# Performance work log

Measured on AMD Instinct MI355X. Metric: run time of the kernel, lower is better.

## Reference

```python
import jax, jax.numpy as jnp
import numpy as np

N_BLOCKS = 2
C = 64
N_HEADS = 4
FF = 256
NB_SEQ = 40
SEQ_LEN = 512
NB_PAIRS = (NB_SEQ * (NB_SEQ - 1)) // 2  # 780
B = 2
EPS_ATT = 1e-6


def _ln(x, g, b, eps=1e-5):
    # LayerNorm over last axis (channels)
    mu = jnp.mean(x, axis=-1, keepdims=True)
    var = jnp.var(x, axis=-1, keepdims=True)
    return (x - mu) * jax.lax.rsqrt(var + eps) * g + b


def _kernel_attn(x, wq, bq, wk, bk, wv, bv, wp, bp):
    # x: [B, M, T, C]; faithful to KernelAxialMultiAttention.
    Bs, M, T, Cc = x.shape
    N, D = N_HEADS, Cc // N_HEADS
    q = jax.nn.elu(x @ wq.T + bq) + 1.0
    k = jax.nn.elu(x @ wk.T + bk) + 1.0
    v = x @ wv.T + bv
    q = q.reshape(Bs, M, T, N, D)
    k = k.reshape(Bs, M, T, N, D)
    v = v.reshape(Bs, M, T, N, D)
    ksum = k.sum(axis=2)                                   # [B,M,N,D]
    z = 1.0 / (jnp.einsum('bmtnd,bmnd->bmtn', q, ksum) + EPS_ATT)  # [B,M,T,N]
    ktv = jnp.einsum('bmtnd,bmtne->bmnde', k, v)           # [B,M,N,D,D]
    # Original does Z.expand(...,T,D) @ KtV where Z's D columns are identical,
    # which equals z * column-sum of KtV (sum over first D axis).
    ktv_cs = ktv.sum(axis=-2)                              # [B,M,N,D]
    V = z[..., None] * ktv_cs[:, :, None, :, :]            # [B,M,T,N,D]
    V = V.reshape(Bs, M, T, Cc)
    return V @ wp.T + bp


def setup_inputs() -> dict:
    key = jax.random.key(0)
    ks = iter(jax.random.split(key, 64))

    def w(shape, scale=0.05):
        return jax.random.normal(next(ks), shape, dtype=jnp.float32) * scale

    # seq2pair gather matrix [P, S]
    ii, jj = np.triu_indices(NB_SEQ, 1)
    sp = np.zeros((NB_PAIRS, NB_SEQ), np.float32)
    sp[np.arange(NB_PAIRS), ii] = 1.0
    sp[np.arange(NB_PAIRS), jj] = 1.0

    inp = {
        'x': jax.random.normal(next(ks), (B, 22, SEQ_LEN, NB_SEQ), dtype=jnp.float32),
        'w_in': w((C, 22)), 'b_in': jnp.zeros((C,), jnp.float32),
        'g0': jnp.ones((C,), jnp.float32), 'be0': jnp.zeros((C,), jnp.float32),
        'rqw': w((N_BLOCKS, C, C)), 'rqb': jnp.zeros((N_BLOCKS, C), jnp.float32),
        'rkw': w((N_BLOCKS, C, C)), 'rkb': jnp.zeros((N_BLOCKS, C), jnp.float32),
        'rvw': w((N_BLOCKS, C, C)), 'rvb': jnp.zeros((N_BLOCKS, C), jnp.float32),
        'rpw': w((N_BLOCKS, C, C)), 'rpb': jnp.zeros((N_BLOCKS, C), jnp.float32),
        'cqw': w((N_BLOCKS, C, C)), 'cqb': jnp.zeros((N_BLOCKS, C), jnp.float32),
        'ckw': w((N_BLOCKS, C, C)), 'ckb': jnp.zeros((N_BLOCKS, C), jnp.float32),
        'cvw': w((N_BLOCKS, C, C)), 'cvb': jnp.zeros((N_BLOCKS, C), jnp.float32),
        'cpw': w((N_BLOCKS, C, C)), 'cpb': jnp.zeros((N_BLOCKS, C), jnp.float32),
        'ln_g': jnp.ones((N_BLOCKS, C), jnp.float32), 'ln_b': jnp.zeros((N_BLOCKS, C), jnp.float32),
        'f1w': w((N_BLOCKS, FF, C)), 'f1b': jnp.zeros((N_BLOCKS, FF), jnp.float32),
        'f2w': w((N_BLOCKS, C, FF)), 'f2b': jnp.zeros((N_BLOCKS, C), jnp.float32),
        'wout': w((1, C)), 'bout': jnp.zeros((1,), jnp.float32),
        'seq2pair': jnp.asarray(sp),
    }
    return inp


def reference(x, w_in, b_in, g0, be0, rqw, rqb, rkw, rkb, rvw, rvb, rpw, rpb,
              cqw, cqb, ckw, ckb, cvw, cvb, cpw, cpb, ln_g, ln_b,
              f1w, f1b, f2w, f2b, wout, bout, seq2pair):
    # block_1_1: 1x1 conv (22->64) + ReLU; x: [B,22,L,S] -> h: [B,C,L,S]
    h = jax.nn.relu(jnp.einsum('bcls,dc->bdls', x, w_in) + b_in[None, :, None, None])
    # seq2pair gather-sum: [B,P,L,C] channel-last representation
    hp = jnp.einsum('ps,bdls->bpld', seq2pair, h)
    hp = _ln(hp, g0, be0)
    for i in range(N_BLOCKS):
        # row attention over seq_len axis (M=P, T=L)
        att = _kernel_attn(hp, rqw[i], rqb[i], rkw[i], rkb[i], rvw[i], rvb[i], rpw[i], rpb[i])
        hp = att + hp
        hp = _ln(hp, ln_g[i], ln_b[i])
        # column attention over pairs axis (M=L, T=P)
        hc = jnp.swapaxes(hp, 1, 2)  # [B,L,P,C]
        att = _kernel_attn(hc, cqw[i], cqb[i], ckw[i], ckb[i], cvw[i], cvb[i], cpw[i], cpb[i])
        hp = jnp.swapaxes(att, 1, 2) + hp
        hp = _ln(hp, ln_g[i], ln_b[i])
        # FFN: 1x1 conv 64->256 GELU 256->64, residual
        f = jax.nn.gelu(hp @ f1w[i].T + f1b[i], approximate=False)
        hp = (f @ f2w[i].T + f2b[i]) + hp
        if i != N_BLOCKS - 1:
            hp = _ln(hp, ln_g[i], ln_b[i])
    # pwFNN: 1x1 conv 64->1 + Softplus, then mean over seq_len axis
    y = jax.nn.softplus(hp @ wout.T + bout)[..., 0]   # [B,P,L]
    return jnp.mean(y, axis=-1)                        # [B,P]
```

## Files before the change

kernel.cpp:

```cpp
#include <hip/hip_runtime.h>
#include <math.h>
#include <stdint.h>

#define B_   2
#define S_   40
#define P_   780
#define L_   512
#define C_   64
#define FF_  256
#define NTOK (B_*P_*L_)

typedef __attribute__((ext_vector_type(8))) short short8;
typedef __attribute__((ext_vector_type(4))) float f32x4;
typedef __attribute__((ext_vector_type(4))) unsigned short us4;

__device__ __forceinline__ float ln64(float r, float g, float b) {
    float s1 = r, s2 = r * r;
    #pragma unroll
    for (int m = 1; m < 64; m <<= 1) {
        s1 += __shfl_xor(s1, m, 64);
        s2 += __shfl_xor(s2, m, 64);
    }
    float mu  = s1 * (1.0f / 64.0f);
    float var = s2 * (1.0f / 64.0f) - mu * mu;
    return (r - mu) * rsqrtf(var + 1e-5f) * g + b;
}
__device__ __forceinline__ float gelu_fast(float x) {
    float x2 = x * x;
    float u  = x * fmaf(0.044715f, x2, 1.0f);
    float e  = __builtin_amdgcn_exp2f(u * 2.302265106f);
    return x * e * __builtin_amdgcn_rcpf(e + 1.0f);
}
__device__ __forceinline__ float softplus_f(float v) {
    return (v > 20.0f) ? v : log1pf(__expf(v));
}
__device__ __forceinline__ float elup1(float v) {
    return (v > 0.0f) ? v + 1.0f : __expf(v);
}
__device__ __forceinline__ unsigned short f2bf(float f) {
    union { float f; uint32_t u; } cv; cv.f = f;
    uint32_t u = cv.u;
    return (unsigned short)((u + 0x7FFFu + ((u >> 16) & 1u)) >> 16);
}
__device__ __forceinline__ float bf2f(unsigned short u) {
    union { uint32_t u; float f; } cv; cv.u = (uint32_t)u << 16; return cv.f;
}
__device__ __forceinline__ uint32_t cvtpk(float a, float b) {
    uint32_t d;
    asm("v_cvt_pk_bf16_f32 %0, %1, %2" : "=v"(d) : "v"(a), "v"(b));
    return d;
}

__global__ void k_conv_in(const float* __restrict__ x, const float* __restrict__ w_in,
                          const float* __restrict__ b_in, float* __restrict__ h) {
    int gid = blockIdx.x * 256 + threadIdx.x;
    int c  = gid & 63;
    int tk = gid >> 6;
    if (tk >= B_ * L_ * S_) return;
    int b = tk / (L_ * S_);
    int r = tk % (L_ * S_);
    int l = r / S_;
    int s = r % S_;
    float acc = b_in[c];
    const float* xb = x + (size_t)b * 22 * L_ * S_ + (size_t)l * S_ + s;
    #pragma unroll
    for (int cc = 0; cc < 22; cc++)
        acc = fmaf(xb[(size_t)cc * L_ * S_], w_in[c * 22 + cc], acc);
    h[gid] = fmaxf(acc, 0.0f);
}

__global__ void k_gather_ln(const float* __restrict__ h, const float* __restrict__ g0,
                            const float* __restrict__ be0, unsigned short* __restrict__ hp) {
    int lane = threadIdx.x & 63;
    int wv   = threadIdx.x >> 6;
    int tk = blockIdx.x * 4 + wv;
    if (tk >= NTOK) return;
    int b = tk / (P_ * L_);
    int r = tk % (P_ * L_);
    int p = r / L_;
    int l = r % L_;
    int i = 0, rem = p, cnt = S_ - 1;
    while (rem >= cnt) { rem -= cnt; cnt--; i++; }
    int j = i + 1 + rem;
    const float* hb = h + (((size_t)b * L_ + l) * S_) * 64;
    float v = hb[i * 64 + lane] + hb[j * 64 + lane];
    hp[(size_t)tk * 64 + lane] = f2bf(ln64(v, g0[lane], be0[lane]));
}

__global__ void k_wprep_qkv(const float* __restrict__ rqw, const float* __restrict__ rkw,
                            const float* __restrict__ rvw, const float* __restrict__ cqw,
                            const float* __restrict__ ckw, const float* __restrict__ cvw,
                            unsigned short* __restrict__ qkvf) {
    int g = blockIdx.x * 256 + threadIdx.x;
    if (g >= 6144) return;
    int m = g >> 9, r = g & 511;
    int mat = m >> 1, layer = m & 1;
    int q = r >> 6, lane = r & 63;
    int c = lane & 15, hi = lane >> 4;
    int nt = q >> 1, s = q & 1;
    const float* base;
    switch (mat) {
        case 0: base = rqw; break; case 1: base = rkw; break; case 2: base = rvw; break;
        case 3: base = cqw; break; case 4: base = ckw; break; default: base = cvw; break;
    }
    const float* src = base + layer * 4096 + (nt * 16 + c) * 64 + s * 32 + hi * 8;
    short8 v;
    #pragma unroll
    for (int i = 0; i < 8; i++) v[i] = (short)f2bf(src[i]);
    *(short8*)(qkvf + (size_t)m * 4096 + (size_t)r * 8) = v;
}

template <bool ROW>
__global__ __launch_bounds__(512) void k_attn_red(
        const unsigned short* __restrict__ xb, const unsigned short* __restrict__ wkf,
        const unsigned short* __restrict__ wvf, const float* __restrict__ bk,
        const float* __restrict__ bv, const float* __restrict__ wp,
        float* __restrict__ stats) {
    __shared__ float redK[8][64];
    __shared__ float redV[8][64];
    __shared__ float kvfin[64];

    const int tid = threadIdx.x, lane = tid & 63, w8 = tid >> 6;
    const int t = lane & 15, hi = lane >> 4;
    const int slice = blockIdx.x;
    const int T  = ROW ? L_ : P_;
    const int NT = ROW ? 32 : 49;
    const size_t base = (size_t)slice * (size_t)T * 64;

    short8 wkfr[4][2], wvfr[4][2];
    #pragma unroll
    for (int nt = 0; nt < 4; nt++)
        #pragma unroll
        for (int s = 0; s < 2; s++) {
            wkfr[nt][s] = *(const short8*)(wkf + ((size_t)((nt*2+s)*64 + lane)) * 8);
            wvfr[nt][s] = *(const short8*)(wvf + ((size_t)((nt*2+s)*64 + lane)) * 8);
        }
    f32x4 bkL[4], bvL[4];
    #pragma unroll
    for (int nt = 0; nt < 4; nt++) {
        bkL[nt] = *(const f32x4*)(bk + nt * 16 + hi * 4);
        bvL[nt] = *(const f32x4*)(bv + nt * 16 + hi * 4);
    }

    float ks[4][4] = {}, kv[4][4] = {};

    for (int tile = w8; tile < NT; tile += 8) {
        int tok = tile * 16 + t;
        bool valid = ROW || (tok < T);
        int tokc = valid ? tok : (T - 1);
        const unsigned short* src = xb + base + (size_t)tokc * 64;
        short8 xf[2];
        #pragma unroll
        for (int s = 0; s < 2; s++)
            xf[s] = *(const short8*)(src + s * 32 + hi * 8);
        f32x4 aK[4], aV[4];
        #pragma unroll
        for (int nt = 0; nt < 4; nt++) { aK[nt] = (f32x4){0,0,0,0}; aV[nt] = (f32x4){0,0,0,0}; }
        #pragma unroll
        for (int nt = 0; nt < 4; nt++)
            #pragma unroll
            for (int s = 0; s < 2; s++) {
                aK[nt] = __builtin_amdgcn_mfma_f32_16x16x32_bf16(wkfr[nt][s], xf[s], aK[nt], 0, 0, 0);
                aV[nt] = __builtin_amdgcn_mfma_f32_16x16x32_bf16(wvfr[nt][s], xf[s], aV[nt], 0, 0, 0);
            }
        #pragma unroll
        for (int nt = 0; nt < 4; nt++) {
            float kk[4], vv[4];
            #pragma unroll
            for (int r = 0; r < 4; r++) {
                kk[r] = valid ? elup1(aK[nt][r] + bkL[nt][r]) : 0.0f;
                vv[r] = valid ? (aV[nt][r] + bvL[nt][r]) : 0.0f;
            }
            float sp = kk[0] + kk[1] + kk[2] + kk[3];
            sp += __shfl_xor(sp, 16, 64);
            sp += __shfl_xor(sp, 32, 64);
            #pragma unroll
            for (int r = 0; r < 4; r++) { ks[nt][r] += kk[r]; kv[nt][r] += sp * vv[r]; }
        }
    }

    #pragma unroll
    for (int nt = 0; nt < 4; nt++)
        #pragma unroll
        for (int r = 0; r < 4; r++) {
            #pragma unroll
            for (int m = 1; m < 16; m <<= 1) {
                ks[nt][r] += __shfl_xor(ks[nt][r], m, 64);
                kv[nt][r] += __shfl_xor(kv[nt][r], m, 64);
            }
        }
    if (t == 0) {
        #pragma unroll
        for (int nt = 0; nt < 4; nt++)
            #pragma unroll
            for (int r = 0; r < 4; r++) {
                redK[w8][nt * 16 + hi * 4 + r] = ks[nt][r];
                redV[w8][nt * 16 + hi * 4 + r] = kv[nt][r];
            }
    }
    __syncthreads();
    if (tid < 64) {
        float a = 0.0f, b2 = 0.0f;
        #pragma unroll
        for (int w = 0; w < 8; w++) { a += redK[w][tid]; b2 += redV[w][tid]; }
        stats[(size_t)slice * 320 + tid] = a;
        kvfin[tid] = b2;
    }
    __syncthreads();
    if (tid < 256) {
        int c = tid & 63, n = tid >> 6;
        const float* wpr = wp + c * 64 + n * 16;
        float s = 0.0f;
        #pragma unroll
        for (int e = 0; e < 16; e++) s = fmaf(kvfin[n * 16 + e], wpr[e], s);
        stats[(size_t)slice * 320 + 64 + c * 4 + n] = s;
    }
}

__global__ __launch_bounds__(256) void k_attn_map_row(
        const unsigned short* __restrict__ hp, unsigned short* __restrict__ hpT,
        const unsigned short* __restrict__ wqf,
        const float* __restrict__ bq, const float* __restrict__ bp,
        const float* __restrict__ stats, const float* __restrict__ lng,
        const float* __restrict__ lnb) {
    const int tid = threadIdx.x, lane = tid & 63, w4 = tid >> 6;
    const int t = lane & 15, hi = lane >> 4;
    const int slice = blockIdx.x >> 3;
    const int tok = ((blockIdx.x & 7) * 4 + w4) * 16 + t;
    const unsigned short* src = hp + ((size_t)slice * L_ + tok) * 64;

    short8 xf[2];
    #pragma unroll
    for (int s = 0; s < 2; s++)
        xf[s] = *(const short8*)(src + s * 32 + hi * 8);

    f32x4 aQ[4];
    #pragma unroll
    for (int nt = 0; nt < 4; nt++) aQ[nt] = (f32x4){0,0,0,0};
    #pragma unroll
    for (int nt = 0; nt < 4; nt++)
        #pragma unroll
        for (int s = 0; s < 2; s++) {
            short8 wfr = *(const short8*)(wqf + ((size_t)((nt*2+s)*64 + lane)) * 8);
            aQ[nt] = __builtin_amdgcn_mfma_f32_16x16x32_bf16(wfr, xf[s], aQ[nt], 0, 0, 0);
        }

    const float* st = stats + (size_t)slice * 320;
    float z[4];
    #pragma unroll
    for (int nt = 0; nt < 4; nt++) {
        f32x4 bq4 = *(const f32x4*)(bq + nt * 16 + hi * 4);
        f32x4 kS  = *(const f32x4*)(st + nt * 16 + hi * 4);
        float d = 0.0f;
        #pragma unroll
        for (int r = 0; r < 4; r++)
            d = fmaf(elup1(aQ[nt][r] + bq4[r]), kS[r], d);
        d += __shfl_xor(d, 16, 64);
        d += __shfl_xor(d, 32, 64);
        z[nt] = 1.0f / (d + 1e-6f);
    }

    float o[4][4];
    float s1 = 0.0f, s2 = 0.0f;
    #pragma unroll
    for (int nt = 0; nt < 4; nt++) {
        f32x4 bp4 = *(const f32x4*)(bp + nt * 16 + hi * 4);
        us4 xr4 = *(const us4*)(src + nt * 16 + hi * 4);
        #pragma unroll
        for (int r = 0; r < 4; r++) {
            int ch = nt * 16 + hi * 4 + r;
            f32x4 wv4 = *(const f32x4*)(st + 64 + ch * 4);
            float val = z[0] * wv4[0] + z[1] * wv4[1] + z[2] * wv4[2] + z[3] * wv4[3]
                      + bp4[r] + bf2f(xr4[r]);
            o[nt][r] = val;
            s1 += val; s2 += val * val;
        }
    }
    s1 += __shfl_xor(s1, 16, 64);  s1 += __shfl_xor(s1, 32, 64);
    s2 += __shfl_xor(s2, 16, 64);  s2 += __shfl_xor(s2, 32, 64);
    float mu  = s1 * (1.0f / 64.0f);
    float var = s2 * (1.0f / 64.0f) - mu * mu;
    float rs  = rsqrtf(var + 1e-5f);

    const int b = slice / P_, p = slice - b * P_;
    unsigned short* dst = hpT + (((size_t)b * L_ + tok) * P_ + p) * 64;
    #pragma unroll
    for (int nt = 0; nt < 4; nt++) {
        f32x4 g4 = *(const f32x4*)(lng + nt * 16 + hi * 4);
        f32x4 b4 = *(const f32x4*)(lnb + nt * 16 + hi * 4);
        float r0 = (o[nt][0] - mu) * rs * g4[0] + b4[0];
        float r1 = (o[nt][1] - mu) * rs * g4[1] + b4[1];
        float r2 = (o[nt][2] - mu) * rs * g4[2] + b4[2];
        float r3 = (o[nt][3] - mu) * rs * g4[3] + b4[3];
        *(uint2*)(dst + nt * 16 + hi * 4) = make_uint2(cvtpk(r0, r1), cvtpk(r2, r3));
    }
}

__global__ void k_wprep(const float* __restrict__ f1w, const float* __restrict__ f2w,
                        unsigned short* __restrict__ w1s, unsigned short* __restrict__ w2s) {
    int g = blockIdx.x * 256 + threadIdx.x;
    if (g >= 8192) return;
    int layer = g >> 12;
    int rem   = g & 4095;
    int which = rem >> 11;
    int idx   = rem & 2047;
    int l  = idx & 63;
    int q  = idx >> 6;
    int c  = l & 15, hi = l >> 4;
    const float* src;
    unsigned short* dst;
    if (which == 0) {
        int s = q & 1, nt = q >> 1;
        src = f1w + (size_t)layer * 16384 + (nt * 16 + c) * 64 + s * 32 + hi * 8;
        dst = w1s + (size_t)layer * 16384 + (size_t)idx * 8;
    } else {
        int s = q & 7, nt = q >> 3;
        src = f2w + (size_t)layer * 16384 + (nt * 16 + c) * 256 + s * 32 + hi * 8;
        dst = w2s + (size_t)layer * 16384 + (size_t)idx * 8;
    }
    short8 v;
    #pragma unroll
    for (int i = 0; i < 8; i++) v[i] = (short)f2bf(src[i]);
    *(short8*)dst = v;
}

template <int MODE>
__global__ __launch_bounds__(256) void k_cmap_ffn(
        const unsigned short* __restrict__ hpT, unsigned short* __restrict__ hp,
        const unsigned short* __restrict__ wqf,
        const float* __restrict__ bq, const float* __restrict__ bpv,
        const float* __restrict__ stats,
        const unsigned short* __restrict__ w1s, const float* __restrict__ f1b,
        const unsigned short* __restrict__ w2s, const float* __restrict__ f2b,
        const float* __restrict__ lng, const float* __restrict__ lnb,
        const float* __restrict__ wout, const float* __restrict__ bout,
        float* __restrict__ out) {
    __shared__ __align__(16) unsigned char Ylds[4][2048];
    __shared__ __align__(16) unsigned char G2[4][4096];

    const int tid = threadIdx.x, lane = tid & 63, wv = tid >> 6;
    const int c = lane & 15, hi = lane >> 4;
    const int slice = blockIdx.x / 13, tile = blockIdx.x % 13;
    const int b = slice >> 9, l = slice & 511;
    const int p = (tile * 4 + wv) * 16 + c;
    const bool valid = p < P_;
    const int pc = valid ? p : P_ - 1;
    const unsigned short* src = hpT + ((size_t)slice * P_ + pc) * 64;

    short8 xf[2];
    #pragma unroll
    for (int s = 0; s < 2; s++)
        xf[s] = *(const short8*)(src + s * 32 + hi * 8);
    f32x4 aQ[4];
    #pragma unroll
    for (int nt = 0; nt < 4; nt++) aQ[nt] = (f32x4){0,0,0,0};
    #pragma unroll
    for (int nt = 0; nt < 4; nt++)
        #pragma unroll
        for (int s = 0; s < 2; s++) {
            short8 wfr = *(const short8*)(wqf + ((size_t)((nt*2+s)*64 + lane)) * 8);
            aQ[nt] = __builtin_amdgcn_mfma_f32_16x16x32_bf16(wfr, xf[s], aQ[nt], 0, 0, 0);
        }
    const float* st = stats + (size_t)slice * 320;
    float z[4];
    #pragma unroll
    for (int nt = 0; nt < 4; nt++) {
        f32x4 bq4 = *(const f32x4*)(bq + nt * 16 + hi * 4);
        f32x4 kS  = *(const f32x4*)(st + nt * 16 + hi * 4);
        float d = 0.0f;
        #pragma unroll
        for (int r = 0; r < 4; r++)
            d = fmaf(elup1(aQ[nt][r] + bq4[r]), kS[r], d);
        d += __shfl_xor(d, 16, 64);
        d += __shfl_xor(d, 32, 64);
        z[nt] = 1.0f / (d + 1e-6f);
    }

    float vv[4][4];
    {
        float s1 = 0.0f, s2 = 0.0f;
        #pragma unroll
        for (int nt = 0; nt < 4; nt++) {
            f32x4 bp4 = *(const f32x4*)(bpv + nt * 16 + hi * 4);
            us4 xr4 = *(const us4*)(src + nt * 16 + hi * 4);
            #pragma unroll
            for (int r = 0; r < 4; r++) {
                int ch = nt * 16 + hi * 4 + r;
                f32x4 wv4 = *(const f32x4*)(st + 64 + ch * 4);
                float val = z[0] * wv4[0] + z[1] * wv4[1] + z[2] * wv4[2] + z[3] * wv4[3]
                          + bp4[r] + bf2f(xr4[r]);
                vv[nt][r] = val;
                s1 += val; s2 += val * val;
            }
        }
        s1 += __shfl_xor(s1, 16, 64);  s1 += __shfl_xor(s1, 32, 64);
        s2 += __shfl_xor(s2, 16, 64);  s2 += __shfl_xor(s2, 32, 64);
        float mu  = s1 * (1.0f / 64.0f);
        float var = s2 * (1.0f / 64.0f) - mu * mu;
        float rs  = rsqrtf(var + 1e-5f);
        #pragma unroll
        for (int nt = 0; nt < 4; nt++) {
            f32x4 g4 = *(const f32x4*)(lng + nt * 16 + hi * 4);
            f32x4 b4 = *(const f32x4*)(lnb + nt * 16 + hi * 4);
            #pragma unroll
            for (int r = 0; r < 4; r++)
                vv[nt][r] = (vv[nt][r] - mu) * rs * g4[r] + b4[r];
        }
    }

    unsigned char* yw = &Ylds[wv][0];
    #pragma unroll
    for (int nt = 0; nt < 4; nt++) {
        uint2 w = make_uint2(cvtpk(vv[nt][0], vv[nt][1]), cvtpk(vv[nt][2], vv[nt][3]));
        uint32_t ch0 = nt * 16 + hi * 4;
        uint32_t boff = (uint32_t)c * 128 + ((ch0 >> 3) ^ (uint32_t)(c & 7)) * 16 + (ch0 & 7) * 2;
        *(uint2*)(yw + boff) = w;
    }
    short8 xb2[2];
    #pragma unroll
    for (int s = 0; s < 2; s++)
        xb2[s] = *(short8*)(yw + (uint32_t)c * 128 +
                            (((uint32_t)(s * 4 + hi)) ^ (uint32_t)(c & 7)) * 16);

    f32x4 acc2[4];
    #pragma unroll
    for (int n2 = 0; n2 < 4; n2++)
        acc2[n2] = *(const f32x4*)(f2b + n2 * 16 + hi * 4);

    unsigned char* g2w = &G2[wv][0] + c * 256;
    #pragma unroll
    for (int half = 0; half < 2; half++) {
        #pragma unroll
        for (int ntl = 0; ntl < 8; ntl++) {
            int nt = half * 8 + ntl;
            f32x4 acc = *(const f32x4*)(f1b + nt * 16 + hi * 4);
            #pragma unroll
            for (int s = 0; s < 2; s++) {
                short8 wf = *(const short8*)(w1s + ((size_t)(nt * 2 + s) * 64 + lane) * 8);
                acc = __builtin_amdgcn_mfma_f32_16x16x32_bf16(wf, xb2[s], acc, 0, 0, 0);
            }
            uint32_t p0 = cvtpk(gelu_fast(acc[0]), gelu_fast(acc[1]));
            uint32_t p1 = cvtpk(gelu_fast(acc[2]), gelu_fast(acc[3]));
            uint32_t woff = ((uint32_t)(ntl * 32 + hi * 8)) ^ ((uint32_t)(c & 7) << 4);
            *(uint2*)(g2w + woff) = make_uint2(p0, p1);
        }
        #pragma unroll
        for (int sl = 0; sl < 4; sl++) {
            int s = half * 4 + sl;
            uint32_t roff = ((uint32_t)(sl * 64 + hi * 16)) ^ ((uint32_t)(c & 7) << 4);
            short8 fa = *(short8*)(g2w + roff);
            #pragma unroll
            for (int n2 = 0; n2 < 4; n2++) {
                short8 wf = *(const short8*)(w2s + ((size_t)(n2 * 8 + s) * 64 + lane) * 8);
                acc2[n2] = __builtin_amdgcn_mfma_f32_16x16x32_bf16(wf, fa, acc2[n2], 0, 0, 0);
            }
        }
    }

    float vo[4][4];
    float s1 = 0.0f, s2 = 0.0f;
    #pragma unroll
    for (int n2 = 0; n2 < 4; n2++)
        #pragma unroll
        for (int r = 0; r < 4; r++) {
            float v = acc2[n2][r] + vv[n2][r];
            vo[n2][r] = v;
            s1 += v; s2 += v * v;
        }

    if (MODE == 0) {
        s1 += __shfl_xor(s1, 16, 64);  s1 += __shfl_xor(s1, 32, 64);
        s2 += __shfl_xor(s2, 16, 64);  s2 += __shfl_xor(s2, 32, 64);
        float mu  = s1 * (1.0f / 64.0f);
        float var = s2 * (1.0f / 64.0f) - mu * mu;
        float rs  = rsqrtf(var + 1e-5f);
        if (valid) {
            unsigned short* dst = hp + (((size_t)b * P_ + pc) * L_ + l) * 64;
            #pragma unroll
            for (int n2 = 0; n2 < 4; n2++) {
                f32x4 g4 = *(const f32x4*)(lng + n2 * 16 + hi * 4);
                f32x4 b4 = *(const f32x4*)(lnb + n2 * 16 + hi * 4);
                float r0 = (vo[n2][0] - mu) * rs * g4[0] + b4[0];
                float r1 = (vo[n2][1] - mu) * rs * g4[1] + b4[1];
                float r2 = (vo[n2][2] - mu) * rs * g4[2] + b4[2];
                float r3 = (vo[n2][3] - mu) * rs * g4[3] + b4[3];
                *(uint2*)(dst + n2 * 16 + hi * 4) = make_uint2(cvtpk(r0, r1), cvtpk(r2, r3));
            }
        }
    } else {
        float part = 0.0f;
        #pragma unroll
        for (int n2 = 0; n2 < 4; n2++) {
            f32x4 w4 = *(const f32x4*)(wout + n2 * 16 + hi * 4);
            #pragma unroll
            for (int r = 0; r < 4; r++)
                part = fmaf(vo[n2][r], w4[r], part);
        }
        part += __shfl_xor(part, 16, 64);
        part += __shfl_xor(part, 32, 64);
        if (hi == 0 && valid) {
            float sp = softplus_f(part + bout[0]);
            atomicAdd(out + b * P_ + pc, sp * (1.0f / L_));
        }
    }
}

extern "C" void kernel_launch(void* const* d_in, const int* in_sizes, int n_in,
                              void* d_out, int out_size, void* d_ws, size_t ws_size,
                              hipStream_t stream) {
    const float* x    = (const float*)d_in[0];
    const float* w_in = (const float*)d_in[1];
    const float* b_in = (const float*)d_in[2];
    const float* g0   = (const float*)d_in[3];
    const float* be0  = (const float*)d_in[4];
    const float* rqw  = (const float*)d_in[5];  const float* rqb = (const float*)d_in[6];
    const float* rkw  = (const float*)d_in[7];  const float* rkb = (const float*)d_in[8];
    const float* rvw  = (const float*)d_in[9];  const float* rvb = (const float*)d_in[10];
    const float* rpw  = (const float*)d_in[11]; const float* rpb = (const float*)d_in[12];
    const float* cqw  = (const float*)d_in[13]; const float* cqb = (const float*)d_in[14];
    const float* ckw  = (const float*)d_in[15]; const float* ckb = (const float*)d_in[16];
    const float* cvw  = (const float*)d_in[17]; const float* cvb = (const float*)d_in[18];
    const float* cpw  = (const float*)d_in[19]; const float* cpb = (const float*)d_in[20];
    const float* lng  = (const float*)d_in[21]; const float* lnb = (const float*)d_in[22];
    const float* f1w  = (const float*)d_in[23]; const float* f1b = (const float*)d_in[24];
    const float* f2w  = (const float*)d_in[25]; const float* f2b = (const float*)d_in[26];
    const float* wout = (const float*)d_in[27]; const float* bout= (const float*)d_in[28];
    float* out = (float*)d_out;

    unsigned short* hp  = (unsigned short*)d_ws;
    unsigned short* hpT = hp + (size_t)NTOK * 64;
    float* h = (float*)(hpT + (size_t)NTOK * 64);
    unsigned short* w1s  = (unsigned short*)h;
    unsigned short* w2s  = w1s + 2 * 16384;
    unsigned short* qkvf = w2s + 2 * 16384;
    float* stats = (float*)(qkvf + 12 * 4096);

    hipMemsetAsync(out, 0, (size_t)out_size * sizeof(float), stream);

    k_conv_in<<<(B_ * L_ * S_ * 64) / 256, 256, 0, stream>>>(x, w_in, b_in, h);
    k_gather_ln<<<NTOK / 4, 256, 0, stream>>>(h, g0, be0, hp);
    k_wprep<<<32, 256, 0, stream>>>(f1w, f2w, w1s, w2s);
    k_wprep_qkv<<<24, 256, 0, stream>>>(rqw, rkw, rvw, cqw, ckw, cvw, qkvf);

    for (int i = 0; i < 2; i++) {
        k_attn_red<true><<<B_ * P_, 512, 0, stream>>>(hp,
            qkvf + (size_t)(2 + i) * 4096, qkvf + (size_t)(4 + i) * 4096,
            rkb + i * 64, rvb + i * 64, rpw + i * 4096, stats);
        k_attn_map_row<<<B_ * P_ * 8, 256, 0, stream>>>(hp, hpT,
            qkvf + (size_t)(0 + i) * 4096, rqb + i * 64, rpb + i * 64,
            stats, lng + i * 64, lnb + i * 64);
        k_attn_red<false><<<B_ * L_, 512, 0, stream>>>(hpT,
            qkvf + (size_t)(8 + i) * 4096, qkvf + (size_t)(10 + i) * 4096,
            ckb + i * 64, cvb + i * 64, cpw + i * 4096, stats);
        if (i == 0) {
            k_cmap_ffn<0><<<B_ * L_ * 13, 256, 0, stream>>>(hpT, hp,
                qkvf + (size_t)(6 + i) * 4096, cqb + i * 64, cpb + i * 64, stats,
                w1s + (size_t)i * 16384, f1b + i * 256,
                w2s + (size_t)i * 16384, f2b + i * 64,
                lng + i * 64, lnb + i * 64, wout, bout, out);
        } else {
            k_cmap_ffn<1><<<B_ * L_ * 13, 256, 0, stream>>>(hpT, hp,
                qkvf + (size_t)(6 + i) * 4096, cqb + i * 64, cpb + i * 64, stats,
                w1s + (size_t)i * 16384, f1b + i * 256,
                w2s + (size_t)i * 16384, f2b + i * 64,
                lng + i * 64, lnb + i * 64, wout, bout, out);
        }
    }
}
```

Before: 1.175 ms.

## Fuse attention reduction and map passes into single per-slice kernels

Merges the K/V reduction kernel with the Q map kernel for row attention, and the column reduction with the column map plus FFN kernel. Each block now owns a whole slice: it keeps the token fragments in registers (row) or re-reads them (column), reduces the stats into shared memory, and applies the map in the same launch. This removes the global stats round trip, two launches per layer, and a second read of the activations. In exchange, grids become much smaller (1560 and 1024 blocks of 512 threads), register and LDS pressure rises, and each block serializes its reduce and map phases.

```diff
diff --git a/kernel.cpp b/kernel.cpp
--- a/kernel.cpp
+++ b/kernel.cpp
@@ -108,192 +108,6 @@
     #pragma unroll
     for (int i = 0; i < 8; i++) v[i] = (short)f2bf(src[i]);
     *(short8*)(qkvf + (size_t)m * 4096 + (size_t)r * 8) = v;
-}
-
-template <bool ROW>
-__global__ __launch_bounds__(512) void k_attn_red(
-        const unsigned short* __restrict__ xb, const unsigned short* __restrict__ wkf,
-        const unsigned short* __restrict__ wvf, const float* __restrict__ bk,
-        const float* __restrict__ bv, const float* __restrict__ wp,
-        float* __restrict__ stats) {
-    __shared__ float redK[8][64];
-    __shared__ float redV[8][64];
-    __shared__ float kvfin[64];
-
-    const int tid = threadIdx.x, lane = tid & 63, w8 = tid >> 6;
-    const int t = lane & 15, hi = lane >> 4;
-    const int slice = blockIdx.x;
-    const int T  = ROW ? L_ : P_;
-    const int NT = ROW ? 32 : 49;
-    const size_t base = (size_t)slice * (size_t)T * 64;
-
-    short8 wkfr[4][2], wvfr[4][2];
-    #pragma unroll
-    for (int nt = 0; nt < 4; nt++)
-        #pragma unroll
-        for (int s = 0; s < 2; s++) {
-            wkfr[nt][s] = *(const short8*)(wkf + ((size_t)((nt*2+s)*64 + lane)) * 8);
-            wvfr[nt][s] = *(const short8*)(wvf + ((size_t)((nt*2+s)*64 + lane)) * 8);
-        }
-    f32x4 bkL[4], bvL[4];
-    #pragma unroll
-    for (int nt = 0; nt < 4; nt++) {
-        bkL[nt] = *(const f32x4*)(bk + nt * 16 + hi * 4);
-        bvL[nt] = *(const f32x4*)(bv + nt * 16 + hi * 4);
-    }
-
-    float ks[4][4] = {}, kv[4][4] = {};
-
-    for (int tile = w8; tile < NT; tile += 8) {
-        int tok = tile * 16 + t;
-        bool valid = ROW || (tok < T);
-        int tokc = valid ? tok : (T - 1);
-        const unsigned short* src = xb + base + (size_t)tokc * 64;
-        short8 xf[2];
-        #pragma unroll
-        for (int s = 0; s < 2; s++)
-            xf[s] = *(const short8*)(src + s * 32 + hi * 8);
-        f32x4 aK[4], aV[4];
-        #pragma unroll
-        for (int nt = 0; nt < 4; nt++) { aK[nt] = (f32x4){0,0,0,0}; aV[nt] = (f32x4){0,0,0,0}; }
-        #pragma unroll
-        for (int nt = 0; nt < 4; nt++)
-            #pragma unroll
-            for (int s = 0; s < 2; s++) {
-                aK[nt] = __builtin_amdgcn_mfma_f32_16x16x32_bf16(wkfr[nt][s], xf[s], aK[nt], 0, 0, 0);
-                aV[nt] = __builtin_amdgcn_mfma_f32_16x16x32_bf16(wvfr[nt][s], xf[s], aV[nt], 0, 0, 0);
-            }
-        #pragma unroll
-        for (int nt = 0; nt < 4; nt++) {
-            float kk[4], vv[4];
-            #pragma unroll
-            for (int r = 0; r < 4; r++) {
-                kk[r] = valid ? elup1(aK[nt][r] + bkL[nt][r]) : 0.0f;
-                vv[r] = valid ? (aV[nt][r] + bvL[nt][r]) : 0.0f;
-            }
-            float sp = kk[0] + kk[1] + kk[2] + kk[3];
-            sp += __shfl_xor(sp, 16, 64);
-            sp += __shfl_xor(sp, 32, 64);
-            #pragma unroll
-            for (int r = 0; r < 4; r++) { ks[nt][r] += kk[r]; kv[nt][r] += sp * vv[r]; }
-        }
-    }
-
-    #pragma unroll
-    for (int nt = 0; nt < 4; nt++)
-        #pragma unroll
-        for (int r = 0; r < 4; r++) {
-            #pragma unroll
-            for (int m = 1; m < 16; m <<= 1) {
-                ks[nt][r] += __shfl_xor(ks[nt][r], m, 64);
-                kv[nt][r] += __shfl_xor(kv[nt][r], m, 64);
-            }
-        }
-    if (t == 0) {
-        #pragma unroll
-        for (int nt = 0; nt < 4; nt++)
-            #pragma unroll
-            for (int r = 0; r < 4; r++) {
-                redK[w8][nt * 16 + hi * 4 + r] = ks[nt][r];
-                redV[w8][nt * 16 + hi * 4 + r] = kv[nt][r];
-            }
-    }
-    __syncthreads();
-    if (tid < 64) {
-        float a = 0.0f, b2 = 0.0f;
-        #pragma unroll
-        for (int w = 0; w < 8; w++) { a += redK[w][tid]; b2 += redV[w][tid]; }
-        stats[(size_t)slice * 320 + tid] = a;
-        kvfin[tid] = b2;
-    }
-    __syncthreads();
-    if (tid < 256) {
-        int c = tid & 63, n = tid >> 6;
-        const float* wpr = wp + c * 64 + n * 16;
-        float s = 0.0f;
-        #pragma unroll
-        for (int e = 0; e < 16; e++) s = fmaf(kvfin[n * 16 + e], wpr[e], s);
-        stats[(size_t)slice * 320 + 64 + c * 4 + n] = s;
-    }
-}
-
-__global__ __launch_bounds__(256) void k_attn_map_row(
-        const unsigned short* __restrict__ hp, unsigned short* __restrict__ hpT,
-        const unsigned short* __restrict__ wqf,
-        const float* __restrict__ bq, const float* __restrict__ bp,
-        const float* __restrict__ stats, const float* __restrict__ lng,
-        const float* __restrict__ lnb) {
-    const int tid = threadIdx.x, lane = tid & 63, w4 = tid >> 6;
-    const int t = lane & 15, hi = lane >> 4;
-    const int slice = blockIdx.x >> 3;
-    const int tok = ((blockIdx.x & 7) * 4 + w4) * 16 + t;
-    const unsigned short* src = hp + ((size_t)slice * L_ + tok) * 64;
-
-    short8 xf[2];
-    #pragma unroll
-    for (int s = 0; s < 2; s++)
-        xf[s] = *(const short8*)(src + s * 32 + hi * 8);
-
-    f32x4 aQ[4];
-    #pragma unroll
-    for (int nt = 0; nt < 4; nt++) aQ[nt] = (f32x4){0,0,0,0};
-    #pragma unroll
-    for (int nt = 0; nt < 4; nt++)
-        #pragma unroll
-        for (int s = 0; s < 2; s++) {
-            short8 wfr = *(const short8*)(wqf + ((size_t)((nt*2+s)*64 + lane)) * 8);
-            aQ[nt] = __builtin_amdgcn_mfma_f32_16x16x32_bf16(wfr, xf[s], aQ[nt], 0, 0, 0);
-        }
-
-    const float* st = stats + (size_t)slice * 320;
-    float z[4];
-    #pragma unroll
-    for (int nt = 0; nt < 4; nt++) {
-        f32x4 bq4 = *(const f32x4*)(bq + nt * 16 + hi * 4);
-        f32x4 kS  = *(const f32x4*)(st + nt * 16 + hi * 4);
-        float d = 0.0f;
-        #pragma unroll
-        for (int r = 0; r < 4; r++)
-            d = fmaf(elup1(aQ[nt][r] + bq4[r]), kS[r], d);
-        d += __shfl_xor(d, 16, 64);
-        d += __shfl_xor(d, 32, 64);
-        z[nt] = 1.0f / (d + 1e-6f);
-    }
-
-    float o[4][4];
-    float s1 = 0.0f, s2 = 0.0f;
-    #pragma unroll
-    for (int nt = 0; nt < 4; nt++) {
-        f32x4 bp4 = *(const f32x4*)(bp + nt * 16 + hi * 4);
-        us4 xr4 = *(const us4*)(src + nt * 16 + hi * 4);
-        #pragma unroll
-        for (int r = 0; r < 4; r++) {
-            int ch = nt * 16 + hi * 4 + r;
-            f32x4 wv4 = *(const f32x4*)(st + 64 + ch * 4);
-            float val = z[0] * wv4[0] + z[1] * wv4[1] + z[2] * wv4[2] + z[3] * wv4[3]
-                      + bp4[r] + bf2f(xr4[r]);
-            o[nt][r] = val;
-            s1 += val; s2 += val * val;
-        }
-    }
-    s1 += __shfl_xor(s1, 16, 64);  s1 += __shfl_xor(s1, 32, 64);
-    s2 += __shfl_xor(s2, 16, 64);  s2 += __shfl_xor(s2, 32, 64);
-    float mu  = s1 * (1.0f / 64.0f);
-    float var = s2 * (1.0f / 64.0f) - mu * mu;
-    float rs  = rsqrtf(var + 1e-5f);
-
-    const int b = slice / P_, p = slice - b * P_;
-    unsigned short* dst = hpT + (((size_t)b * L_ + tok) * P_ + p) * 64;
-    #pragma unroll
-    for (int nt = 0; nt < 4; nt++) {
-        f32x4 g4 = *(const f32x4*)(lng + nt * 16 + hi * 4);
-        f32x4 b4 = *(const f32x4*)(lnb + nt * 16 + hi * 4);
-        float r0 = (o[nt][0] - mu) * rs * g4[0] + b4[0];
-        float r1 = (o[nt][1] - mu) * rs * g4[1] + b4[1];
-        float r2 = (o[nt][2] - mu) * rs * g4[2] + b4[2];
-        float r3 = (o[nt][3] - mu) * rs * g4[3] + b4[3];
-        *(uint2*)(dst + nt * 16 + hi * 4) = make_uint2(cvtpk(r0, r1), cvtpk(r2, r3));
-    }
 }
 
 __global__ void k_wprep(const float* __restrict__ f1w, const float* __restrict__ f2w,
@@ -324,183 +138,464 @@
     *(short8*)dst = v;
 }
 
+__global__ __launch_bounds__(512) void k_row_fused(
+        const unsigned short* __restrict__ hp, unsigned short* __restrict__ hpT,
+        const unsigned short* __restrict__ wqf, const unsigned short* __restrict__ wkf,
+        const unsigned short* __restrict__ wvf,
+        const float* __restrict__ bq, const float* __restrict__ bk,
+        const float* __restrict__ bv, const float* __restrict__ wp,
+        const float* __restrict__ bp, const float* __restrict__ lng,
+        const float* __restrict__ lnb) {
+    __shared__ float redK[8][64];
+    __shared__ float redV[8][64];
+    __shared__ float kvfin[64];
+    __shared__ float sksum[64];
+    __shared__ float swkv[256];
+
+    const int tid = threadIdx.x, lane = tid & 63, w8 = tid >> 6;
+    const int t = lane & 15, hi = lane >> 4;
+    const int slice = blockIdx.x;
+    const size_t base = (size_t)slice * L_ * 64;
+
+    short8 xkeep[4][2];
+    float ks[4][4] = {}, kv[4][4] = {};
+    {
+        short8 wkfr[4][2], wvfr[4][2];
+        #pragma unroll
+        for (int nt = 0; nt < 4; nt++)
+            #pragma unroll
+            for (int s = 0; s < 2; s++) {
+                wkfr[nt][s] = *(const short8*)(wkf + ((size_t)((nt*2+s)*64 + lane)) * 8);
+                wvfr[nt][s] = *(const short8*)(wvf + ((size_t)((nt*2+s)*64 + lane)) * 8);
+            }
+        f32x4 bkL[4], bvL[4];
+        #pragma unroll
+        for (int nt = 0; nt < 4; nt++) {
+            bkL[nt] = *(const f32x4*)(bk + nt * 16 + hi * 4);
+            bvL[nt] = *(const f32x4*)(bv + nt * 16 + hi * 4);
+        }
+        #pragma unroll
+        for (int it = 0; it < 4; it++) {
+            int tok = (w8 + it * 8) * 16 + t;
+            const unsigned short* src = hp + base + (size_t)tok * 64;
+            #pragma unroll
+            for (int s = 0; s < 2; s++)
+                xkeep[it][s] = *(const short8*)(src + s * 32 + hi * 8);
+            f32x4 aK[4], aV[4];
+            #pragma unroll
+            for (int nt = 0; nt < 4; nt++) { aK[nt] = (f32x4){0,0,0,0}; aV[nt] = (f32x4){0,0,0,0}; }
+            #pragma unroll
+            for (int nt = 0; nt < 4; nt++)
+                #pragma unroll
+                for (int s = 0; s < 2; s++) {
+                    aK[nt] = __builtin_amdgcn_mfma_f32_16x16x32_bf16(wkfr[nt][s], xkeep[it][s], aK[nt], 0, 0, 0);
+                    aV[nt] = __builtin_amdgcn_mfma_f32_16x16x32_bf16(wvfr[nt][s], xkeep[it][s], aV[nt], 0, 0, 0);
+                }
+            #pragma unroll
+            for (int nt = 0; nt < 4; nt++) {
+                float kk[4], vv[4];
+                #pragma unroll
+                for (int r = 0; r < 4; r++) {
+                    kk[r] = elup1(aK[nt][r] + bkL[nt][r]);
+                    vv[r] = aV[nt][r] + bvL[nt][r];
+                }
+                float sp = kk[0] + kk[1] + kk[2] + kk[3];
+                sp += __shfl_xor(sp, 16, 64);
+                sp += __shfl_xor(sp, 32, 64);
+                #pragma unroll
+                for (int r = 0; r < 4; r++) { ks[nt][r] += kk[r]; kv[nt][r] += sp * vv[r]; }
+            }
+        }
+    }
+    #pragma unroll
+    for (int nt = 0; nt < 4; nt++)
+        #pragma unroll
+        for (int r = 0; r < 4; r++) {
+            #pragma unroll
+            for (int m = 1; m < 16; m <<= 1) {
+                ks[nt][r] += __shfl_xor(ks[nt][r], m, 64);
+                kv[nt][r] += __shfl_xor(kv[nt][r], m, 64);
+            }
+        }
+    if (t == 0) {
+        #pragma unroll
+        for (int nt = 0; nt < 4; nt++)
+            #pragma unroll
+            for (int r = 0; r < 4; r++) {
+                redK[w8][nt * 16 + hi * 4 + r] = ks[nt][r];
+                redV[w8][nt * 16 + hi * 4 + r] = kv[nt][r];
+            }
+    }
+    __syncthreads();
+    if (tid < 64) {
+        float a = 0.0f, b2 = 0.0f;
+        #pragma unroll
+        for (int w = 0; w < 8; w++) { a += redK[w][tid]; b2 += redV[w][tid]; }
+        sksum[tid] = a;
+        kvfin[tid] = b2;
+    }
+    __syncthreads();
+    if (tid < 256) {
+        int c = tid & 63, n = tid >> 6;
+        const float* wpr = wp + c * 64 + n * 16;
+        float s = 0.0f;
+        #pragma unroll
+        for (int e = 0; e < 16; e++) s = fmaf(kvfin[n * 16 + e], wpr[e], s);
+        swkv[c * 4 + n] = s;
+    }
+    __syncthreads();
+
+    short8 wqfr[4][2];
+    #pragma unroll
+    for (int nt = 0; nt < 4; nt++)
+        #pragma unroll
+        for (int s = 0; s < 2; s++)
+            wqfr[nt][s] = *(const short8*)(wqf + ((size_t)((nt*2+s)*64 + lane)) * 8);
+    f32x4 bqL[4], bpL[4], gL[4], bL[4];
+    #pragma unroll
+    for (int nt = 0; nt < 4; nt++) {
+        bqL[nt] = *(const f32x4*)(bq + nt * 16 + hi * 4);
+        bpL[nt] = *(const f32x4*)(bp + nt * 16 + hi * 4);
+        gL[nt]  = *(const f32x4*)(lng + nt * 16 + hi * 4);
+        bL[nt]  = *(const f32x4*)(lnb + nt * 16 + hi * 4);
+    }
+    const int bb = slice / P_, pp = slice - bb * P_;
+
+    #pragma unroll
+    for (int it = 0; it < 4; it++) {
+        int tok = (w8 + it * 8) * 16 + t;
+        f32x4 aQ[4];
+        #pragma unroll
+        for (int nt = 0; nt < 4; nt++) aQ[nt] = (f32x4){0,0,0,0};
+        #pragma unroll
+        for (int nt = 0; nt < 4; nt++)
+            #pragma unroll
+            for (int s = 0; s < 2; s++)
+                aQ[nt] = __builtin_amdgcn_mfma_f32_16x16x32_bf16(wqfr[nt][s], xkeep[it][s], aQ[nt], 0, 0, 0);
+        float z[4];
+        #pragma unroll
+        for (int nt = 0; nt < 4; nt++) {
+            f32x4 kS = *(const f32x4*)(sksum + nt * 16 + hi * 4);
+            float d = 0.0f;
+            #pragma unroll
+            for (int r = 0; r < 4; r++)
+                d = fmaf(elup1(aQ[nt][r] + bqL[nt][r]), kS[r], d);
+            d += __shfl_xor(d, 16, 64);
+            d += __shfl_xor(d, 32, 64);
+            z[nt] = 1.0f / (d + 1e-6f);
+        }
+        const unsigned short* srcr = hp + base + (size_t)tok * 64;
+        float o[4][4];
+        float s1 = 0.0f, s2 = 0.0f;
+        #pragma unroll
+        for (int nt = 0; nt < 4; nt++) {
+            us4 xr4 = *(const us4*)(srcr + nt * 16 + hi * 4);
+            #pragma unroll
+            for (int r = 0; r < 4; r++) {
+                int ch = nt * 16 + hi * 4 + r;
+                f32x4 wv4 = *(const f32x4*)(swkv + ch * 4);
+                float val = z[0] * wv4[0] + z[1] * wv4[1] + z[2] * wv4[2] + z[3] * wv4[3]
+                          + bpL[nt][r] + bf2f(xr4[r]);
+                o[nt][r] = val;
+                s1 += val; s2 += val * val;
+            }
+        }
+        s1 += __shfl_xor(s1, 16, 64);  s1 += __shfl_xor(s1, 32, 64);
+        s2 += __shfl_xor(s2, 16, 64);  s2 += __shfl_xor(s2, 32, 64);
+        float mu  = s1 * (1.0f / 64.0f);
+        float var = s2 * (1.0f / 64.0f) - mu * mu;
+        float rs  = rsqrtf(var + 1e-5f);
+        unsigned short* dst = hpT + (((size_t)bb * L_ + tok) * P_ + pp) * 64;
+        #pragma unroll
+        for (int nt = 0; nt < 4; nt++) {
+            float r0 = (o[nt][0] - mu) * rs * gL[nt][0] + bL[nt][0];
+            float r1 = (o[nt][1] - mu) * rs * gL[nt][1] + bL[nt][1];
+            float r2 = (o[nt][2] - mu) * rs * gL[nt][2] + bL[nt][2];
+            float r3 = (o[nt][3] - mu) * rs * gL[nt][3] + bL[nt][3];
+            *(uint2*)(dst + nt * 16 + hi * 4) = make_uint2(cvtpk(r0, r1), cvtpk(r2, r3));
+        }
+    }
+}
+
 template <int MODE>
-__global__ __launch_bounds__(256) void k_cmap_ffn(
+__global__ __launch_bounds__(512) void k_col_fused(
         const unsigned short* __restrict__ hpT, unsigned short* __restrict__ hp,
-        const unsigned short* __restrict__ wqf,
-        const float* __restrict__ bq, const float* __restrict__ bpv,
-        const float* __restrict__ stats,
+        const unsigned short* __restrict__ wqf, const unsigned short* __restrict__ wkf,
+        const unsigned short* __restrict__ wvf,
+        const float* __restrict__ bq, const float* __restrict__ bk,
+        const float* __restrict__ bv, const float* __restrict__ wp,
+        const float* __restrict__ bpv,
         const unsigned short* __restrict__ w1s, const float* __restrict__ f1b,
         const unsigned short* __restrict__ w2s, const float* __restrict__ f2b,
         const float* __restrict__ lng, const float* __restrict__ lnb,
         const float* __restrict__ wout, const float* __restrict__ bout,
         float* __restrict__ out) {
-    __shared__ __align__(16) unsigned char Ylds[4][2048];
-    __shared__ __align__(16) unsigned char G2[4][4096];
-
-    const int tid = threadIdx.x, lane = tid & 63, wv = tid >> 6;
-    const int c = lane & 15, hi = lane >> 4;
-    const int slice = blockIdx.x / 13, tile = blockIdx.x % 13;
-    const int b = slice >> 9, l = slice & 511;
-    const int p = (tile * 4 + wv) * 16 + c;
-    const bool valid = p < P_;
-    const int pc = valid ? p : P_ - 1;
-    const unsigned short* src = hpT + ((size_t)slice * P_ + pc) * 64;
-
-    short8 xf[2];
-    #pragma unroll
-    for (int s = 0; s < 2; s++)
-        xf[s] = *(const short8*)(src + s * 32 + hi * 8);
-    f32x4 aQ[4];
-    #pragma unroll
-    for (int nt = 0; nt < 4; nt++) aQ[nt] = (f32x4){0,0,0,0};
+    __shared__ float redK[8][64];
+    __shared__ float redV[8][64];
+    __shared__ float kvfin[64];
+    __shared__ float sksum[64];
+    __shared__ float swkv[256];
+    __shared__ __align__(16) unsigned char G2[8][4096];
+
+    const int tid = threadIdx.x, lane = tid & 63, w8 = tid >> 6;
+    const int t = lane & 15, hi = lane >> 4;
+    const int slice = blockIdx.x;
+    const int bb = slice >> 9, ll = slice & 511;
+    const size_t base = (size_t)slice * P_ * 64;
+
+    float ks[4][4] = {}, kv[4][4] = {};
+    {
+        short8 wkfr[4][2], wvfr[4][2];
+        #pragma unroll
+        for (int nt = 0; nt < 4; nt++)
+            #pragma unroll
+            for (int s = 0; s < 2; s++) {
+                wkfr[nt][s] = *(const short8*)(wkf + ((size_t)((nt*2+s)*64 + lane)) * 8);
+                wvfr[nt][s] = *(const short8*)(wvf + ((size_t)((nt*2+s)*64 + lane)) * 8);
+            }
+        f32x4 bkL[4], bvL[4];
+        #pragma unroll
+        for (int nt = 0; nt < 4; nt++) {
+            bkL[nt] = *(const f32x4*)(bk + nt * 16 + hi * 4);
+            bvL[nt] = *(const f32x4*)(bv + nt * 16 + hi * 4);
+        }
+        #pragma unroll 1
+        for (int tile = w8; tile < 49; tile += 8) {
+            int tok = tile * 16 + t;
+            bool valid = tok < P_;
+            int tokc = valid ? tok : (P_ - 1);
+            const unsigned short* src = hpT + base + (size_t)tokc * 64;
+            short8 xf[2];
+            #pragma unroll
+            for (int s = 0; s < 2; s++)
+                xf[s] = *(const short8*)(src + s * 32 + hi * 8);
+            f32x4 aK[4], aV[4];
+            #pragma unroll
+            for (int nt = 0; nt < 4; nt++) { aK[nt] = (f32x4){0,0,0,0}; aV[nt] = (f32x4){0,0,0,0}; }
+            #pragma unroll
+            for (int nt = 0; nt < 4; nt++)
+                #pragma unroll
+                for (int s = 0; s < 2; s++) {
+                    aK[nt] = __builtin_amdgcn_mfma_f32_16x16x32_bf16(wkfr[nt][s], xf[s], aK[nt], 0, 0, 0);
+                    aV[nt] = __builtin_amdgcn_mfma_f32_16x16x32_bf16(wvfr[nt][s], xf[s], aV[nt], 0, 0, 0);
+                }
+            #pragma unroll
+            for (int nt = 0; nt < 4; nt++) {
+                float kk[4], vv[4];
+                #pragma unroll
+                for (int r = 0; r < 4; r++) {
+                    kk[r] = valid ? elup1(aK[nt][r] + bkL[nt][r]) : 0.0f;
+                    vv[r] = valid ? (aV[nt][r] + bvL[nt][r]) : 0.0f;
+                }
+                float sp = kk[0] + kk[1] + kk[2] + kk[3];
+                sp += __shfl_xor(sp, 16, 64);
+                sp += __shfl_xor(sp, 32, 64);
+                #pragma unroll
+                for (int r = 0; r < 4; r++) { ks[nt][r] += kk[r]; kv[nt][r] += sp * vv[r]; }
+            }
+        }
+    }
     #pragma unroll
     for (int nt = 0; nt < 4; nt++)
         #pragma unroll
-        for (int s = 0; s < 2; s++) {
-            short8 wfr = *(const short8*)(wqf + ((size_t)((nt*2+s)*64 + lane)) * 8);
-            aQ[nt] = __builtin_amdgcn_mfma_f32_16x16x32_bf16(wfr, xf[s], aQ[nt], 0, 0, 0);
-        }
-    const float* st = stats + (size_t)slice * 320;
-    float z[4];
+        for (int r = 0; r < 4; r++) {
+            #pragma unroll
+            for (int m = 1; m < 16; m <<= 1) {
+                ks[nt][r] += __shfl_xor(ks[nt][r], m, 64);
+                kv[nt][r] += __shfl_xor(kv[nt][r], m, 64);
+            }
+        }
+    if (t == 0) {
+        #pragma unroll
+        for (int nt = 0; nt < 4; nt++)
+            #pragma unroll
+            for (int r = 0; r < 4; r++) {
+                redK[w8][nt * 16 + hi * 4 + r] = ks[nt][r];
+                redV[w8][nt * 16 + hi * 4 + r] = kv[nt][r];
+            }
+    }
+    __syncthreads();
+    if (tid < 64) {
+        float a = 0.0f, b2 = 0.0f;
+        #pragma unroll
+        for (int w = 0; w < 8; w++) { a += redK[w][tid]; b2 += redV[w][tid]; }
+        sksum[tid] = a;
+        kvfin[tid] = b2;
+    }
+    __syncthreads();
+    if (tid < 256) {
+        int c = tid & 63, n = tid >> 6;
+        const float* wpr = wp + c * 64 + n * 16;
+        float s = 0.0f;
+        #pragma unroll
+        for (int e = 0; e < 16; e++) s = fmaf(kvfin[n * 16 + e], wpr[e], s);
+        swkv[c * 4 + n] = s;
+    }
+    __syncthreads();
+
+    short8 wqfr[4][2];
+    #pragma unroll
+    for (int nt = 0; nt < 4; nt++)
+        #pragma unroll
+        for (int s = 0; s < 2; s++)
+            wqfr[nt][s] = *(const short8*)(wqf + ((size_t)((nt*2+s)*64 + lane)) * 8);
+    f32x4 bqL[4], bpL[4], gL[4], bL[4], f2bL[4];
     #pragma unroll
     for (int nt = 0; nt < 4; nt++) {
-        f32x4 bq4 = *(const f32x4*)(bq + nt * 16 + hi * 4);
-        f32x4 kS  = *(const f32x4*)(st + nt * 16 + hi * 4);
-        float d = 0.0f;
-        #pragma unroll
-        for (int r = 0; r < 4; r++)
-            d = fmaf(elup1(aQ[nt][r] + bq4[r]), kS[r], d);
-        d += __shfl_xor(d, 16, 64);
-        d += __shfl_xor(d, 32, 64);
-        z[nt] = 1.0f / (d + 1e-6f);
-    }
-
-    float vv[4][4];
-    {
+        bqL[nt]  = *(const f32x4*)(bq  + nt * 16 + hi * 4);
+        bpL[nt]  = *(const f32x4*)(bpv + nt * 16 + hi * 4);
+        gL[nt]   = *(const f32x4*)(lng + nt * 16 + hi * 4);
+        bL[nt]   = *(const f32x4*)(lnb + nt * 16 + hi * 4);
+        f2bL[nt] = *(const f32x4*)(f2b + nt * 16 + hi * 4);
+    }
+    unsigned char* yw  = &G2[w8][0];
+    unsigned char* g2w = &G2[w8][0] + t * 256;
+
+    #pragma unroll 1
+    for (int tile = w8; tile < 49; tile += 8) {
+        int p = tile * 16 + t;
+        bool valid = p < P_;
+        int pc = valid ? p : P_ - 1;
+        const unsigned short* src = hpT + base + (size_t)pc * 64;
+        short8 xf[2];
+        #pragma unroll
+        for (int s = 0; s < 2; s++)
+            xf[s] = *(const short8*)(src + s * 32 + hi * 8);
+        f32x4 aQ[4];
+        #pragma unroll
+        for (int nt = 0; nt < 4; nt++) aQ[nt] = (f32x4){0,0,0,0};
+        #pragma unroll
+        for (int nt = 0; nt < 4; nt++)
+            #pragma unroll
+            for (int s = 0; s < 2; s++)
+                aQ[nt] = __builtin_amdgcn_mfma_f32_16x16x32_bf16(wqfr[nt][s], xf[s], aQ[nt], 0, 0, 0);
+        float z[4];
+        #pragma unroll
+        for (int nt = 0; nt < 4; nt++) {
+            f32x4 kS = *(const f32x4*)(sksum + nt * 16 + hi * 4);
+            float d = 0.0f;
+            #pragma unroll
+            for (int r = 0; r < 4; r++)
+                d = fmaf(elup1(aQ[nt][r] + bqL[nt][r]), kS[r], d);
+            d += __shfl_xor(d, 16, 64);
+            d += __shfl_xor(d, 32, 64);
+            z[nt] = 1.0f / (d + 1e-6f);
+        }
+        float vv[4][4];
+        {
+            float s1 = 0.0f, s2 = 0.0f;
+            #pragma unroll
+            for (int nt = 0; nt < 4; nt++) {
+                us4 xr4 = *(const us4*)(src + nt * 16 + hi * 4);
+                #pragma unroll
+                for (int r = 0; r < 4; r++) {
+                    int ch = nt * 16 + hi * 4 + r;
+                    f32x4 wv4 = *(const f32x4*)(swkv + ch * 4);
+                    float val = z[0] * wv4[0] + z[1] * wv4[1] + z[2] * wv4[2] + z[3] * wv4[3]
+                              + bpL[nt][r] + bf2f(xr4[r]);
+                    vv[nt][r] = val;
+                    s1 += val; s2 += val * val;
+                }
+            }
+            s1 += __shfl_xor(s1, 16, 64);  s1 += __shfl_xor(s1, 32, 64);
+            s2 += __shfl_xor(s2, 16, 64);  s2 += __shfl_xor(s2, 32, 64);
+            float mu  = s1 * (1.0f / 64.0f);
+            float var = s2 * (1.0f / 64.0f) - mu * mu;
+            float rs  = rsqrtf(var + 1e-5f);
+            #pragma unroll
+            for (int nt = 0; nt < 4; nt++)
+                #pragma unroll
+                for (int r = 0; r < 4; r++)
+                    vv[nt][r] = (vv[nt][r] - mu) * rs * gL[nt][r] + bL[nt][r];
+        }
+
+        #pragma unroll
+        for (int nt = 0; nt < 4; nt++) {
+            uint2 w = make_uint2(cvtpk(vv[nt][0], vv[nt][1]), cvtpk(vv[nt][2], vv[nt][3]));
+            uint32_t ch0 = nt * 16 + hi * 4;
+            uint32_t boff = (uint32_t)t * 128 + ((ch0 >> 3) ^ (uint32_t)(t & 7)) * 16 + (ch0 & 7) * 2;
+            *(uint2*)(yw + boff) = w;
+        }
+        short8 xb2[2];
+        #pragma unroll
+        for (int s = 0; s < 2; s++)
+            xb2[s] = *(short8*)(yw + (uint32_t)t * 128 +
+                                (((uint32_t)(s * 4 + hi)) ^ (uint32_t)(t & 7)) * 16);
+
+        f32x4 acc2[4];
+        #pragma unroll
+        for (int n2 = 0; n2 < 4; n2++) acc2[n2] = f2bL[n2];
+        #pragma unroll
+        for (int half = 0; half < 2; half++) {
+            #pragma unroll
+            for (int ntl = 0; ntl < 8; ntl++) {
+                int nt = half * 8 + ntl;
+                f32x4 acc = *(const f32x4*)(f1b + nt * 16 + hi * 4);
+                #pragma unroll
+                for (int s = 0; s < 2; s++) {
+                    short8 wf = *(const short8*)(w1s + ((size_t)(nt * 2 + s) * 64 + lane) * 8);
+                    acc = __builtin_amdgcn_mfma_f32_16x16x32_bf16(wf, xb2[s], acc, 0, 0, 0);
+                }
+                uint32_t p0 = cvtpk(gelu_fast(acc[0]), gelu_fast(acc[1]));
+                uint32_t p1 = cvtpk(gelu_fast(acc[2]), gelu_fast(acc[3]));
+                uint32_t woff = ((uint32_t)(ntl * 32 + hi * 8)) ^ ((uint32_t)(t & 7) << 4);
+                *(uint2*)(g2w + woff) = make_uint2(p0, p1);
+            }
+            #pragma unroll
+            for (int sl = 0; sl < 4; sl++) {
+                int s = half * 4 + sl;
+                uint32_t roff = ((uint32_t)(sl * 64 + hi * 16)) ^ ((uint32_t)(t & 7) << 4);
+                short8 fa = *(short8*)(g2w + roff);
+                #pragma unroll
+                for (int n2 = 0; n2 < 4; n2++) {
+                    short8 wf = *(const short8*)(w2s + ((size_t)(n2 * 8 + s) * 64 + lane) * 8);
+                    acc2[n2] = __builtin_amdgcn_mfma_f32_16x16x32_bf16(wf, fa, acc2[n2], 0, 0, 0);
+                }
+            }
+        }
+
+        float vo[4][4];
         float s1 = 0.0f, s2 = 0.0f;
         #pragma unroll
-        for (int nt = 0; nt < 4; nt++) {
-            f32x4 bp4 = *(const f32x4*)(bpv + nt * 16 + hi * 4);
-            us4 xr4 = *(const us4*)(src + nt * 16 + hi * 4);
+        for (int n2 = 0; n2 < 4; n2++)
             #pragma unroll
             for (int r = 0; r < 4; r++) {
-                int ch = nt * 16 + hi * 4 + r;
-                f32x4 wv4 = *(const f32x4*)(st + 64 + ch * 4);
-                float val = z[0] * wv4[0] + z[1] * wv4[1] + z[2] * wv4[2] + z[3] * wv4[3]
-                          + bp4[r] + bf2f(xr4[r]);
-                vv[nt][r] = val;
-                s1 += val; s2 += val * val;
-            }
-        }
-        s1 += __shfl_xor(s1, 16, 64);  s1 += __shfl_xor(s1, 32, 64);
-        s2 += __shfl_xor(s2, 16, 64);  s2 += __shfl_xor(s2, 32, 64);
-        float mu  = s1 * (1.0f / 64.0f);
-        float var = s2 * (1.0f / 64.0f) - mu * mu;
-        float rs  = rsqrtf(var + 1e-5f);
-        #pragma unroll
-        for (int nt = 0; nt < 4; nt++) {
-            f32x4 g4 = *(const f32x4*)(lng + nt * 16 + hi * 4);
-            f32x4 b4 = *(const f32x4*)(lnb + nt * 16 + hi * 4);
-            #pragma unroll
-            for (int r = 0; r < 4; r++)
-                vv[nt][r] = (vv[nt][r] - mu) * rs * g4[r] + b4[r];
-        }
-    }
-
-    unsigned char* yw = &Ylds[wv][0];
-    #pragma unroll
-    for (int nt = 0; nt < 4; nt++) {
-        uint2 w = make_uint2(cvtpk(vv[nt][0], vv[nt][1]), cvtpk(vv[nt][2], vv[nt][3]));
-        uint32_t ch0 = nt * 16 + hi * 4;
-        uint32_t boff = (uint32_t)c * 128 + ((ch0 >> 3) ^ (uint32_t)(c & 7)) * 16 + (ch0 & 7) * 2;
-        *(uint2*)(yw + boff) = w;
-    }
-    short8 xb2[2];
-    #pragma unroll
-    for (int s = 0; s < 2; s++)
-        xb2[s] = *(short8*)(yw + (uint32_t)c * 128 +
-                            (((uint32_t)(s * 4 + hi)) ^ (uint32_t)(c & 7)) * 16);
-
-    f32x4 acc2[4];
-    #pragma unroll
-    for (int n2 = 0; n2 < 4; n2++)
-        acc2[n2] = *(const f32x4*)(f2b + n2 * 16 + hi * 4);
-
-    unsigned char* g2w = &G2[wv][0] + c * 256;
-    #pragma unroll
-    for (int half = 0; half < 2; half++) {
-        #pragma unroll
-        for (int ntl = 0; ntl < 8; ntl++) {
-            int nt = half * 8 + ntl;
-            f32x4 acc = *(const f32x4*)(f1b + nt * 16 + hi * 4);
-            #pragma unroll
-            for (int s = 0; s < 2; s++) {
-                short8 wf = *(const short8*)(w1s + ((size_t)(nt * 2 + s) * 64 + lane) * 8);
-                acc = __builtin_amdgcn_mfma_f32_16x16x32_bf16(wf, xb2[s], acc, 0, 0, 0);
-            }
-            uint32_t p0 = cvtpk(gelu_fast(acc[0]), gelu_fast(acc[1]));
-            uint32_t p1 = cvtpk(gelu_fast(acc[2]), gelu_fast(acc[3]));
-            uint32_t woff = ((uint32_t)(ntl * 32 + hi * 8)) ^ ((uint32_t)(c & 7) << 4);
-            *(uint2*)(g2w + woff) = make_uint2(p0, p1);
-        }
-        #pragma unroll
-        for (int sl = 0; sl < 4; sl++) {
-            int s = half * 4 + sl;
-            uint32_t roff = ((uint32_t)(sl * 64 + hi * 16)) ^ ((uint32_t)(c & 7) << 4);
-            short8 fa = *(short8*)(g2w + roff);
+                float v = acc2[n2][r] + vv[n2][r];
+                vo[n2][r] = v;
+                s1 += v; s2 += v * v;
+            }
+        if (MODE == 0) {
+            s1 += __shfl_xor(s1, 16, 64);  s1 += __shfl_xor(s1, 32, 64);
+            s2 += __shfl_xor(s2, 16, 64);  s2 += __shfl_xor(s2, 32, 64);
+            float mu  = s1 * (1.0f / 64.0f);
+            float var = s2 * (1.0f / 64.0f) - mu * mu;
+            float rs  = rsqrtf(var + 1e-5f);
+            if (valid) {
+                unsigned short* dst = hp + (((size_t)bb * P_ + pc) * L_ + ll) * 64;
+                #pragma unroll
+                for (int n2 = 0; n2 < 4; n2++) {
+                    float r0 = (vo[n2][0] - mu) * rs * gL[n2][0] + bL[n2][0];
+                    float r1 = (vo[n2][1] - mu) * rs * gL[n2][1] + bL[n2][1];
+                    float r2 = (vo[n2][2] - mu) * rs * gL[n2][2] + bL[n2][2];
+                    float r3 = (vo[n2][3] - mu) * rs * gL[n2][3] + bL[n2][3];
+                    *(uint2*)(dst + n2 * 16 + hi * 4) = make_uint2(cvtpk(r0, r1), cvtpk(r2, r3));
+                }
+            }
+        } else {
+            float part = 0.0f;
             #pragma unroll
             for (int n2 = 0; n2 < 4; n2++) {
-                short8 wf = *(const short8*)(w2s + ((size_t)(n2 * 8 + s) * 64 + lane) * 8);
-                acc2[n2] = __builtin_amdgcn_mfma_f32_16x16x32_bf16(wf, fa, acc2[n2], 0, 0, 0);
-            }
-        }
-    }
-
-    float vo[4][4];
-    float s1 = 0.0f, s2 = 0.0f;
-    #pragma unroll
-    for (int n2 = 0; n2 < 4; n2++)
-        #pragma unroll
-        for (int r = 0; r < 4; r++) {
-            float v = acc2[n2][r] + vv[n2][r];
-            vo[n2][r] = v;
-            s1 += v; s2 += v * v;
-        }
-
-    if (MODE == 0) {
-        s1 += __shfl_xor(s1, 16, 64);  s1 += __shfl_xor(s1, 32, 64);
-        s2 += __shfl_xor(s2, 16, 64);  s2 += __shfl_xor(s2, 32, 64);
-        float mu  = s1 * (1.0f / 64.0f);
-        float var = s2 * (1.0f / 64.0f) - mu * mu;
-        float rs  = rsqrtf(var + 1e-5f);
-        if (valid) {
-            unsigned short* dst = hp + (((size_t)b * P_ + pc) * L_ + l) * 64;
-            #pragma unroll
-            for (int n2 = 0; n2 < 4; n2++) {
-                f32x4 g4 = *(const f32x4*)(lng + n2 * 16 + hi * 4);
-                f32x4 b4 = *(const f32x4*)(lnb + n2 * 16 + hi * 4);
-                float r0 = (vo[n2][0] - mu) * rs * g4[0] + b4[0];
-                float r1 = (vo[n2][1] - mu) * rs * g4[1] + b4[1];
-                float r2 = (vo[n2][2] - mu) * rs * g4[2] + b4[2];
-                float r3 = (vo[n2][3] - mu) * rs * g4[3] + b4[3];
-                *(uint2*)(dst + n2 * 16 + hi * 4) = make_uint2(cvtpk(r0, r1), cvtpk(r2, r3));
-            }
-        }
-    } else {
-        float part = 0.0f;
-        #pragma unroll
-        for (int n2 = 0; n2 < 4; n2++) {
-            f32x4 w4 = *(const f32x4*)(wout + n2 * 16 + hi * 4);
-            #pragma unroll
-            for (int r = 0; r < 4; r++)
-                part = fmaf(vo[n2][r], w4[r], part);
-        }
-        part += __shfl_xor(part, 16, 64);
-        part += __shfl_xor(part, 32, 64);
-        if (hi == 0 && valid) {
-            float sp = softplus_f(part + bout[0]);
-            atomicAdd(out + b * P_ + pc, sp * (1.0f / L_));
+                f32x4 w4 = *(const f32x4*)(wout + n2 * 16 + hi * 4);
+                #pragma unroll
+                for (int r = 0; r < 4; r++)
+                    part = fmaf(vo[n2][r], w4[r], part);
+            }
+            part += __shfl_xor(part, 16, 64);
+            part += __shfl_xor(part, 32, 64);
+            if (hi == 0 && valid) {
+                float sp = softplus_f(part + bout[0]);
+                atomicAdd(out + bb * P_ + pc, sp * (1.0f / L_));
+            }
         }
     }
 }
@@ -533,7 +628,6 @@
     unsigned short* w1s  = (unsigned short*)h;
     unsigned short* w2s  = w1s + 2 * 16384;
     unsigned short* qkvf = w2s + 2 * 16384;
-    float* stats = (float*)(qkvf + 12 * 4096);
 
     hipMemsetAsync(out, 0, (size_t)out_size * sizeof(float), stream);
 
@@ -543,24 +637,24 @@
     k_wprep_qkv<<<24, 256, 0, stream>>>(rqw, rkw, rvw, cqw, ckw, cvw, qkvf);
 
     for (int i = 0; i < 2; i++) {
-        k_attn_red<true><<<B_ * P_, 512, 0, stream>>>(hp,
-            qkvf + (size_t)(2 + i) * 4096, qkvf + (size_t)(4 + i) * 4096,
-            rkb + i * 64, rvb + i * 64, rpw + i * 4096, stats);
-        k_attn_map_row<<<B_ * P_ * 8, 256, 0, stream>>>(hp, hpT,
-            qkvf + (size_t)(0 + i) * 4096, rqb + i * 64, rpb + i * 64,
-            stats, lng + i * 64, lnb + i * 64);
-        k_attn_red<false><<<B_ * L_, 512, 0, stream>>>(hpT,
-            qkvf + (size_t)(8 + i) * 4096, qkvf + (size_t)(10 + i) * 4096,
-            ckb + i * 64, cvb + i * 64, cpw + i * 4096, stats);
+        k_row_fused<<<B_ * P_, 512, 0, stream>>>(hp, hpT,
+            qkvf + (size_t)(0 + i) * 4096, qkvf + (size_t)(2 + i) * 4096,
+            qkvf + (size_t)(4 + i) * 4096,
+            rqb + i * 64, rkb + i * 64, rvb + i * 64, rpw + i * 4096, rpb + i * 64,
+            lng + i * 64, lnb + i * 64);
         if (i == 0) {
-            k_cmap_ffn<0><<<B_ * L_ * 13, 256, 0, stream>>>(hpT, hp,
-                qkvf + (size_t)(6 + i) * 4096, cqb + i * 64, cpb + i * 64, stats,
+            k_col_fused<0><<<B_ * L_, 512, 0, stream>>>(hpT, hp,
+                qkvf + (size_t)(6 + i) * 4096, qkvf + (size_t)(8 + i) * 4096,
+                qkvf + (size_t)(10 + i) * 4096,
+                cqb + i * 64, ckb + i * 64, cvb + i * 64, cpw + i * 4096, cpb + i * 64,
                 w1s + (size_t)i * 16384, f1b + i * 256,
                 w2s + (size_t)i * 16384, f2b + i * 64,
                 lng + i * 64, lnb + i * 64, wout, bout, out);
         } else {
-            k_cmap_ffn<1><<<B_ * L_ * 13, 256, 0, stream>>>(hpT, hp,
-                qkvf + (size_t)(6 + i) * 4096, cqb + i * 64, cpb + i * 64, stats,
+            k_col_fused<1><<<B_ * L_, 512, 0, stream>>>(hpT, hp,
+                qkvf + (size_t)(6 + i) * 4096, qkvf + (size_t)(8 + i) * 4096,
+                qkvf + (size_t)(10 + i) * 4096,
+                cqb + i * 64, ckb + i * 64, cvb + i * 64, cpw + i * 4096, cpb + i * 64,
                 w1s + (size_t)i * 16384, f1b + i * 256,
                 w2s + (size_t)i * 16384, f2b + i * 64,
                 lng + i * 64, lnb + i * 64, wout, bout, out);
```

Measured after the change: 2.296 ms. +95.5%, slower.
